# Optimization experiments

Hardware: AMD Instinct MI355X
Metric: run time of the kernel (lower is better)

The kernel has to match this reference:

```python
import jax, jax.numpy as jnp
import numpy as np

B, G, N, C = 8, 16, 1024, 256


def setup_inputs() -> dict:
    key = jax.random.key(0)
    k1, k2, k3, k4, k5 = jax.random.split(key, 5)
    x = jax.random.normal(k1, (B, G, N, C), dtype=jnp.float32)
    vs = jax.random.normal(k2, (B, G, 1, N, 3), dtype=jnp.float32)
    s = 1.0 / np.sqrt(C)
    W_fc = jax.random.normal(k3, (C, C), dtype=jnp.float32) * s   # nn.Linear weight [out,in]
    b_fc = jax.random.normal(k4, (C,), dtype=jnp.float32) * s
    W_vn = jax.random.normal(k5, (C, C), dtype=jnp.float32) * s   # VNLinear weight [out,in], no bias
    return {"x": x, "vs": vs, "W_fc": W_fc, "b_fc": b_fc, "W_vn": W_vn}


def reference(x, vs, W_fc, b_fc, W_vn):
    # q = fc(x): [B,G,N,C]
    q = jnp.einsum('bgnc,oc->bgno', x, W_fc) + b_fc
    # softmax over the point dim N (torch dim=2)
    atten = jax.nn.softmax(q, axis=2)
    xw = atten * x  # [B,G,N,C]
    # torch: expand to [B,G,C,N,3] * vs then sum over N.
    # Equivalent contraction without materializing the 5D tensor:
    v = jnp.squeeze(vs, axis=2)  # [B,G,N,3]
    out = jnp.einsum('bgnc,bgnd->bgcd', xw, v)  # [B,G,C,3]
    # VNLinear: bias-free linear over channel dim, shared across the 3 vector comps
    return jnp.einsum('bgcd,oc->bgod', out, W_vn)  # [B,G,C,3]
```

## Files before the change

### kernel.cpp

```cpp
#include <hip/hip_runtime.h>
#include <hip/hip_bf16.h>


#define NQ 1024
#define CQ 256
#define RT 64
#define XS2 264
#define WB_OFF 131072

typedef __attribute__((ext_vector_type(8))) short bf16x8;
typedef __attribute__((ext_vector_type(4))) float f32x4;

__device__ __forceinline__ ushort2 pk2(float a, float b) {
    __hip_bfloat162 h = __float22bfloat162_rn(make_float2(a, b));
    ushort2 r;
    __builtin_memcpy(&r, &h, sizeof(r));
    return r;
}
__device__ __forceinline__ float bf2f(ushort h) {
    union { unsigned u; float f; } v; v.u = ((unsigned)h) << 16;
    return v.f;
}

__device__ __forceinline__ void bar_lgkm() {
    __builtin_amdgcn_sched_barrier(0);
    asm volatile("s_waitcnt lgkmcnt(0)" ::: "memory");
    __builtin_amdgcn_sched_barrier(0);
    __builtin_amdgcn_s_barrier();
    __builtin_amdgcn_sched_barrier(0);
}

__global__ __launch_bounds__(256)
void wfc_cvt(const float* __restrict__ Wfc, ushort* __restrict__ WbT) {
    const int i = blockIdx.x * 256 + threadIdx.x;
    const int o = i >> 6;
    const int k4 = (i & 63) * 4;
    float4 v = *reinterpret_cast<const float4*>(Wfc + (size_t)o * CQ + k4);
    ushort2 a0 = pk2(v.x, v.y), a1 = pk2(v.z, v.w);
    ushort4 pk = { a0.x, a0.y, a1.x, a1.y };
    *reinterpret_cast<ushort4*>(WbT + ((size_t)(k4 >> 3) * CQ + o) * 8 + (k4 & 7)) = pk;
}

__global__ __launch_bounds__(512, 4)
void attn_pool_partial(const float* __restrict__ x, const float* __restrict__ vs,
                       const ushort* __restrict__ WbT, float* __restrict__ ws) {
    __shared__ __align__(16) ushort xs[RT * XS2];
    __shared__ __align__(16) float  vsm[RT * 3];

    const int t = threadIdx.x;
    const int id = blockIdx.x;
    const int bg = id >> 4;
    const int nt = id & 15;
    const int n0 = nt * RT;

    const int w = t >> 6, lane = t & 63;
    const int quad = lane >> 4, l16 = lane & 15;
    const int bcol0 = w * 32 + l16;

    const float* xb = x + (size_t)bg * NQ * CQ;
    const float* vb = vs + (size_t)bg * NQ * 3;

    const bool vload = (t < 48);
    float4 vreg;
    if (vload) vreg = reinterpret_cast<const float4*>(vb + (size_t)n0 * 3)[t];
    __builtin_amdgcn_sched_barrier(0);

    float4 LA[8];
    #pragma unroll
    for (int p = 0; p < 8; ++p) {
        const int idx = p * 512 + t;
        const int row = idx >> 6, k4 = idx & 63;
        LA[p] = *reinterpret_cast<const float4*>(
            xb + (size_t)(n0 + row) * CQ + k4 * 4);
    }
    __builtin_amdgcn_sched_barrier(0);

    bf16x8 Bf0[8], Bf1[8];
    #pragma unroll
    for (int ks = 0; ks < 8; ++ks) {
        const size_t fo = (size_t)(ks * 4 + quad) * (CQ * 8);
        Bf0[ks] = *reinterpret_cast<const bf16x8*>(WbT + fo + (size_t)bcol0 * 8);
        Bf1[ks] = *reinterpret_cast<const bf16x8*>(WbT + fo + (size_t)(bcol0 + 16) * 8);
    }
    __builtin_amdgcn_sched_barrier(0);

    #pragma unroll
    for (int p = 0; p < 8; ++p) {
        const int idx = p * 512 + t;
        const int row = idx >> 6, k4 = idx & 63;
        ushort2 a0 = pk2(LA[p].x, LA[p].y), a1 = pk2(LA[p].z, LA[p].w);
        ushort4 pk = { a0.x, a0.y, a1.x, a1.y };
        *reinterpret_cast<ushort4*>(&xs[row * XS2 + k4 * 4]) = pk;
    }
    if (vload) reinterpret_cast<float4*>(vsm)[t] = vreg;

    bar_lgkm();

    f32x4 acc[4][2];
    #pragma unroll
    for (int m = 0; m < 4; ++m)
        #pragma unroll
        for (int ci = 0; ci < 2; ++ci) acc[m][ci] = (f32x4){0.f, 0.f, 0.f, 0.f};

    __builtin_amdgcn_s_setprio(1);
    #pragma unroll
    for (int ks = 0; ks < 8; ++ks) {
        const int kk = ks * 32 + quad * 8;
        #pragma unroll
        for (int m = 0; m < 4; ++m) {
            bf16x8 a = *reinterpret_cast<const bf16x8*>(&xs[(m * 16 + l16) * XS2 + kk]);
            acc[m][0] = __builtin_amdgcn_mfma_f32_16x16x32_bf16(a, Bf0[ks], acc[m][0], 0, 0, 0);
            acc[m][1] = __builtin_amdgcn_mfma_f32_16x16x32_bf16(a, Bf1[ks], acc[m][1], 0, 0, 0);
        }
    }
    __builtin_amdgcn_s_setprio(0);

    float rZ[2] = {0.f, 0.f}, rS0[2] = {0.f, 0.f}, rS1[2] = {0.f, 0.f}, rS2[2] = {0.f, 0.f};
    #pragma unroll
    for (int m = 0; m < 4; ++m) {
        const int rbase = m * 16 + quad * 4;
        float v0[4], v1[4], v2[4];
        #pragma unroll
        for (int r = 0; r < 4; ++r) {
            v0[r] = vsm[(rbase + r) * 3 + 0];
            v1[r] = vsm[(rbase + r) * 3 + 1];
            v2[r] = vsm[(rbase + r) * 3 + 2];
        }
        #pragma unroll
        for (int ci = 0; ci < 2; ++ci) {
            const int xc = w * 32 + ci * 16 + l16;
            #pragma unroll
            for (int r = 0; r < 4; ++r) {
                float e = __expf(acc[m][ci][r]);
                float xv = bf2f(xs[(rbase + r) * XS2 + xc]);
                rZ[ci] += e;
                float p = e * xv;
                rS0[ci] = fmaf(p, v0[r], rS0[ci]);
                rS1[ci] = fmaf(p, v1[r], rS1[ci]);
                rS2[ci] = fmaf(p, v2[r], rS2[ci]);
            }
        }
    }

    #pragma unroll
    for (int ci = 0; ci < 2; ++ci) {
        float z = rZ[ci], s0 = rS0[ci], s1 = rS1[ci], s2 = rS2[ci];
        #pragma unroll
        for (int off = 16; off < 64; off <<= 1) {
            z  += __shfl_xor(z,  off);
            s0 += __shfl_xor(s0, off);
            s1 += __shfl_xor(s1, off);
            s2 += __shfl_xor(s2, off);
        }
        if (quad == 0) {
            const int col = w * 32 + ci * 16 + l16;
            float* p = ws + ((size_t)bg * CQ + col) * 4;
            atomicAdd(&p[0], z);
            atomicAdd(&p[1], s0);
            atomicAdd(&p[2], s1);
            atomicAdd(&p[3], s2);
        }
    }
}

__global__ __launch_bounds__(256, 4)
void vn_linear(const float* __restrict__ ws, const float* __restrict__ Wvn,
               float* __restrict__ out) {
    __shared__ float Tsm[CQ][3];
    const int bg = blockIdx.x, t = threadIdx.x;
    {
        f32x4 z4 = *reinterpret_cast<const f32x4*>(ws + ((size_t)bg * CQ + t) * 4);
        float inv = 1.f / z4[0];
        Tsm[t][0] = z4[1] * inv;
        Tsm[t][1] = z4[2] * inv;
        Tsm[t][2] = z4[3] * inv;
    }
    __syncthreads();
    const float* wr = Wvn + (size_t)t * CQ;
    float a0 = 0.f, a1 = 0.f, a2 = 0.f;
    #pragma unroll
    for (int c = 0; c < CQ; c += 4) {
        float4 w4 = *reinterpret_cast<const float4*>(wr + c);
        a0 += w4.x * Tsm[c + 0][0] + w4.y * Tsm[c + 1][0]
            + w4.z * Tsm[c + 2][0] + w4.w * Tsm[c + 3][0];
        a1 += w4.x * Tsm[c + 0][1] + w4.y * Tsm[c + 1][1]
            + w4.z * Tsm[c + 2][1] + w4.w * Tsm[c + 3][1];
        a2 += w4.x * Tsm[c + 0][2] + w4.y * Tsm[c + 1][2]
            + w4.z * Tsm[c + 2][2] + w4.w * Tsm[c + 3][2];
    }
    float* op = out + ((size_t)bg * CQ + t) * 3;
    op[0] = a0; op[1] = a1; op[2] = a2;
}

extern "C" void kernel_launch(void* const* d_in, const int* in_sizes, int n_in,
                              void* d_out, int out_size, void* d_ws, size_t ws_size,
                              hipStream_t stream) {
    const float* x   = (const float*)d_in[0];
    const float* vs  = (const float*)d_in[1];
    const float* Wfc = (const float*)d_in[2];
    const float* Wvn = (const float*)d_in[4];
    float* out = (float*)d_out;
    float* ws  = (float*)d_ws;

    ushort* WbT = (ushort*)(ws + WB_OFF);

    (void)hipMemsetAsync(ws, 0, (size_t)128 * CQ * 4 * sizeof(float), stream);
    wfc_cvt<<<dim3(64), dim3(256), 0, stream>>>(Wfc, WbT);
    attn_pool_partial<<<dim3(2048), dim3(512), 0, stream>>>(x, vs, WbT, ws);
    vn_linear<<<dim3(128), dim3(256), 0, stream>>>(ws, Wvn, out);
}
```

Before: 217.1 us.

## Double-buffer x tiles in LDS and process four row tiles per block

Each block now handles four 64-row tiles of one (b,g) instead of one, with a double-buffered LDS staging area. The next tile's global loads are issued in two halves interleaved with the MFMA and softmax work on the current tile, so memory latency overlaps compute. The W_fc fragments are loaded into registers once per block rather than once per tile, and atomics drop by a factor of four. The trade-off is fewer blocks (512) and doubled LDS, which may reduce occupancy and the latency hiding that came from having many resident blocks.

```diff
diff --git a/kernel.cpp b/kernel.cpp
--- a/kernel.cpp
+++ b/kernel.cpp
@@ -44,36 +44,23 @@
 __global__ __launch_bounds__(512, 4)
 void attn_pool_partial(const float* __restrict__ x, const float* __restrict__ vs,
                        const ushort* __restrict__ WbT, float* __restrict__ ws) {
-    __shared__ __align__(16) ushort xs[RT * XS2];
-    __shared__ __align__(16) float  vsm[RT * 3];
+    __shared__ __align__(16) ushort xs[2][RT * XS2];
+    __shared__ __align__(16) float  vsm[2][RT * 3];
 
     const int t = threadIdx.x;
     const int id = blockIdx.x;
-    const int bg = id >> 4;
-    const int nt = id & 15;
-    const int n0 = nt * RT;
+    const int bg = id >> 2;
+    const int ntg = id & 3;
+    const int nb = ntg * 4 * RT;
 
     const int w = t >> 6, lane = t & 63;
     const int quad = lane >> 4, l16 = lane & 15;
     const int bcol0 = w * 32 + l16;
+    const bool vload = (t < 48);
 
     const float* xb = x + (size_t)bg * NQ * CQ;
     const float* vb = vs + (size_t)bg * NQ * 3;
 
-    const bool vload = (t < 48);
-    float4 vreg;
-    if (vload) vreg = reinterpret_cast<const float4*>(vb + (size_t)n0 * 3)[t];
-    __builtin_amdgcn_sched_barrier(0);
-
-    float4 LA[8];
-    #pragma unroll
-    for (int p = 0; p < 8; ++p) {
-        const int idx = p * 512 + t;
-        const int row = idx >> 6, k4 = idx & 63;
-        LA[p] = *reinterpret_cast<const float4*>(
-            xb + (size_t)(n0 + row) * CQ + k4 * 4);
-    }
-    __builtin_amdgcn_sched_barrier(0);
 
     bf16x8 Bf0[8], Bf1[8];
     #pragma unroll
@@ -84,61 +71,171 @@
     }
     __builtin_amdgcn_sched_barrier(0);
 
+    {
+        float4 vreg;
+        if (vload) vreg = reinterpret_cast<const float4*>(vb + (size_t)nb * 3)[t];
+        float4 L[8];
+        #pragma unroll
+        for (int p = 0; p < 8; ++p) {
+            const int row = p * 8 + w;
+            L[p] = *reinterpret_cast<const float4*>(
+                xb + (size_t)(nb + row) * CQ + lane * 4);
+        }
+        __builtin_amdgcn_sched_barrier(0);
+        #pragma unroll
+        for (int p = 0; p < 8; ++p) {
+            const int row = p * 8 + w;
+            ushort2 a0 = pk2(L[p].x, L[p].y), a1 = pk2(L[p].z, L[p].w);
+            ushort4 pk = { a0.x, a0.y, a1.x, a1.y };
+            *reinterpret_cast<ushort4*>(&xs[0][row * XS2 + lane * 4]) = pk;
+        }
+        if (vload) reinterpret_cast<float4*>(vsm[0])[t] = vreg;
+    }
+    bar_lgkm();
+
+    float rZ[2] = {0.f, 0.f}, rS0[2] = {0.f, 0.f}, rS1[2] = {0.f, 0.f}, rS2[2] = {0.f, 0.f};
+
     #pragma unroll
-    for (int p = 0; p < 8; ++p) {
-        const int idx = p * 512 + t;
-        const int row = idx >> 6, k4 = idx & 63;
-        ushort2 a0 = pk2(LA[p].x, LA[p].y), a1 = pk2(LA[p].z, LA[p].w);
-        ushort4 pk = { a0.x, a0.y, a1.x, a1.y };
-        *reinterpret_cast<ushort4*>(&xs[row * XS2 + k4 * 4]) = pk;
-    }
-    if (vload) reinterpret_cast<float4*>(vsm)[t] = vreg;
-
-    bar_lgkm();
-
-    f32x4 acc[4][2];
-    #pragma unroll
-    for (int m = 0; m < 4; ++m)
-        #pragma unroll
-        for (int ci = 0; ci < 2; ++ci) acc[m][ci] = (f32x4){0.f, 0.f, 0.f, 0.f};
-
-    __builtin_amdgcn_s_setprio(1);
-    #pragma unroll
-    for (int ks = 0; ks < 8; ++ks) {
-        const int kk = ks * 32 + quad * 8;
-        #pragma unroll
-        for (int m = 0; m < 4; ++m) {
-            bf16x8 a = *reinterpret_cast<const bf16x8*>(&xs[(m * 16 + l16) * XS2 + kk]);
-            acc[m][0] = __builtin_amdgcn_mfma_f32_16x16x32_bf16(a, Bf0[ks], acc[m][0], 0, 0, 0);
-            acc[m][1] = __builtin_amdgcn_mfma_f32_16x16x32_bf16(a, Bf1[ks], acc[m][1], 0, 0, 0);
-        }
-    }
-    __builtin_amdgcn_s_setprio(0);
-
-    float rZ[2] = {0.f, 0.f}, rS0[2] = {0.f, 0.f}, rS1[2] = {0.f, 0.f}, rS2[2] = {0.f, 0.f};
-    #pragma unroll
-    for (int m = 0; m < 4; ++m) {
-        const int rbase = m * 16 + quad * 4;
-        float v0[4], v1[4], v2[4];
-        #pragma unroll
-        for (int r = 0; r < 4; ++r) {
-            v0[r] = vsm[(rbase + r) * 3 + 0];
-            v1[r] = vsm[(rbase + r) * 3 + 1];
-            v2[r] = vsm[(rbase + r) * 3 + 2];
-        }
-        #pragma unroll
-        for (int ci = 0; ci < 2; ++ci) {
-            const int xc = w * 32 + ci * 16 + l16;
-            #pragma unroll
-            for (int r = 0; r < 4; ++r) {
-                float e = __expf(acc[m][ci][r]);
-                float xv = bf2f(xs[(rbase + r) * XS2 + xc]);
-                rZ[ci] += e;
-                float p = e * xv;
-                rS0[ci] = fmaf(p, v0[r], rS0[ci]);
-                rS1[ci] = fmaf(p, v1[r], rS1[ci]);
-                rS2[ci] = fmaf(p, v2[r], rS2[ci]);
-            }
+    for (int i = 0; i < 4; ++i) {
+        const int cur = i & 1, nxt = cur ^ 1;
+        const bool pf = (i < 3);
+        const size_t nnb = (size_t)(nb + (i + 1) * RT);
+
+        float4 LAa[4], LAb[4], vreg;
+        if (pf) {
+            if (vload) vreg = reinterpret_cast<const float4*>(vb + nnb * 3)[t];
+            #pragma unroll
+            for (int p = 0; p < 4; ++p) {
+                const int row = p * 8 + w;
+                LAa[p] = *reinterpret_cast<const float4*>(
+                    xb + (nnb + row) * CQ + lane * 4);
+            }
+        }
+        __builtin_amdgcn_sched_barrier(0);
+
+        {
+            f32x4 acc[2][2];
+            #pragma unroll
+            for (int mi = 0; mi < 2; ++mi)
+                #pragma unroll
+                for (int ci = 0; ci < 2; ++ci) acc[mi][ci] = (f32x4){0.f, 0.f, 0.f, 0.f};
+            __builtin_amdgcn_s_setprio(1);
+            #pragma unroll
+            for (int ks = 0; ks < 8; ++ks) {
+                const int kk = ks * 32 + quad * 8;
+                #pragma unroll
+                for (int mi = 0; mi < 2; ++mi) {
+                    bf16x8 a = *reinterpret_cast<const bf16x8*>(
+                        &xs[cur][(mi * 16 + l16) * XS2 + kk]);
+                    acc[mi][0] = __builtin_amdgcn_mfma_f32_16x16x32_bf16(a, Bf0[ks], acc[mi][0], 0, 0, 0);
+                    acc[mi][1] = __builtin_amdgcn_mfma_f32_16x16x32_bf16(a, Bf1[ks], acc[mi][1], 0, 0, 0);
+                }
+            }
+            __builtin_amdgcn_s_setprio(0);
+            #pragma unroll
+            for (int mi = 0; mi < 2; ++mi) {
+                const int rbase = mi * 16 + quad * 4;
+                float v0[4], v1[4], v2[4];
+                #pragma unroll
+                for (int r = 0; r < 4; ++r) {
+                    v0[r] = vsm[cur][(rbase + r) * 3 + 0];
+                    v1[r] = vsm[cur][(rbase + r) * 3 + 1];
+                    v2[r] = vsm[cur][(rbase + r) * 3 + 2];
+                }
+                #pragma unroll
+                for (int ci = 0; ci < 2; ++ci) {
+                    const int xc = w * 32 + ci * 16 + l16;
+                    #pragma unroll
+                    for (int r = 0; r < 4; ++r) {
+                        float e = __expf(acc[mi][ci][r]);
+                        float xv = bf2f(xs[cur][(rbase + r) * XS2 + xc]);
+                        rZ[ci] += e;
+                        float p = e * xv;
+                        rS0[ci] = fmaf(p, v0[r], rS0[ci]);
+                        rS1[ci] = fmaf(p, v1[r], rS1[ci]);
+                        rS2[ci] = fmaf(p, v2[r], rS2[ci]);
+                    }
+                }
+            }
+        }
+
+        if (pf) {
+            #pragma unroll
+            for (int p = 0; p < 4; ++p) {
+                const int row = p * 8 + w;
+                ushort2 a0 = pk2(LAa[p].x, LAa[p].y), a1 = pk2(LAa[p].z, LAa[p].w);
+                ushort4 pk = { a0.x, a0.y, a1.x, a1.y };
+                *reinterpret_cast<ushort4*>(&xs[nxt][row * XS2 + lane * 4]) = pk;
+            }
+            if (vload) reinterpret_cast<float4*>(vsm[nxt])[t] = vreg;
+        }
+        __builtin_amdgcn_sched_barrier(0);
+
+        if (pf) {
+            #pragma unroll
+            for (int p = 0; p < 4; ++p) {
+                const int row = 32 + p * 8 + w;
+                LAb[p] = *reinterpret_cast<const float4*>(
+                    xb + (nnb + row) * CQ + lane * 4);
+            }
+        }
+        __builtin_amdgcn_sched_barrier(0);
+
+        {
+            f32x4 acc[2][2];
+            #pragma unroll
+            for (int mi = 0; mi < 2; ++mi)
+                #pragma unroll
+                for (int ci = 0; ci < 2; ++ci) acc[mi][ci] = (f32x4){0.f, 0.f, 0.f, 0.f};
+            __builtin_amdgcn_s_setprio(1);
+            #pragma unroll
+            for (int ks = 0; ks < 8; ++ks) {
+                const int kk = ks * 32 + quad * 8;
+                #pragma unroll
+                for (int mi = 0; mi < 2; ++mi) {
+                    bf16x8 a = *reinterpret_cast<const bf16x8*>(
+                        &xs[cur][((mi + 2) * 16 + l16) * XS2 + kk]);
+                    acc[mi][0] = __builtin_amdgcn_mfma_f32_16x16x32_bf16(a, Bf0[ks], acc[mi][0], 0, 0, 0);
+                    acc[mi][1] = __builtin_amdgcn_mfma_f32_16x16x32_bf16(a, Bf1[ks], acc[mi][1], 0, 0, 0);
+                }
+            }
+            __builtin_amdgcn_s_setprio(0);
+            #pragma unroll
+            for (int mi = 0; mi < 2; ++mi) {
+                const int rbase = (mi + 2) * 16 + quad * 4;
+                float v0[4], v1[4], v2[4];
+                #pragma unroll
+                for (int r = 0; r < 4; ++r) {
+                    v0[r] = vsm[cur][(rbase + r) * 3 + 0];
+                    v1[r] = vsm[cur][(rbase + r) * 3 + 1];
+                    v2[r] = vsm[cur][(rbase + r) * 3 + 2];
+                }
+                #pragma unroll
+                for (int ci = 0; ci < 2; ++ci) {
+                    const int xc = w * 32 + ci * 16 + l16;
+                    #pragma unroll
+                    for (int r = 0; r < 4; ++r) {
+                        float e = __expf(acc[mi][ci][r]);
+                        float xv = bf2f(xs[cur][(rbase + r) * XS2 + xc]);
+                        rZ[ci] += e;
+                        float p = e * xv;
+                        rS0[ci] = fmaf(p, v0[r], rS0[ci]);
+                        rS1[ci] = fmaf(p, v1[r], rS1[ci]);
+                        rS2[ci] = fmaf(p, v2[r], rS2[ci]);
+                    }
+                }
+            }
+        }
+
+        if (pf) {
+            #pragma unroll
+            for (int p = 0; p < 4; ++p) {
+                const int row = 32 + p * 8 + w;
+                ushort2 a0 = pk2(LAb[p].x, LAb[p].y), a1 = pk2(LAb[p].z, LAb[p].w);
+                ushort4 pk = { a0.x, a0.y, a1.x, a1.y };
+                *reinterpret_cast<ushort4*>(&xs[nxt][row * XS2 + lane * 4]) = pk;
+            }
+            bar_lgkm();
         }
     }
 
@@ -206,6 +303,6 @@
 
     (void)hipMemsetAsync(ws, 0, (size_t)128 * CQ * 4 * sizeof(float), stream);
     wfc_cvt<<<dim3(64), dim3(256), 0, stream>>>(Wfc, WbT);
-    attn_pool_partial<<<dim3(2048), dim3(512), 0, stream>>>(x, vs, WbT, ws);
+    attn_pool_partial<<<dim3(512), dim3(512), 0, stream>>>(x, vs, WbT, ws);
     vn_linear<<<dim3(128), dim3(256), 0, stream>>>(ws, Wvn, out);
 }
```

Result: slower. 368.8 us (+69.9%).

## Double-buffer x tiles via direct global-to-LDS loads in persistent blocks

Applied to the files above, without the earlier changes.

Each block now walks 8 tiles of 32 rows instead of handling one 64-row tile, so the grid shrinks from 2048 to 512 blocks. The x tiles are loaded as fp32 straight into LDS with global_load_lds into a double buffer, using an XOR swizzle, and are converted to bf16 when the MFMA operands are read. The goal is to overlap the HBM loads with compute, skip the register round trip, and load the W_fc fragments once per block rather than once per tile. In exchange it uses twice the LDS (fp32 staging), repeats the bf16 conversion inside the MFMA loop, and leaves fewer blocks to hide latency across the device.

```diff
diff --git a/kernel.cpp b/kernel.cpp
--- a/kernel.cpp
+++ b/kernel.cpp
@@ -4,8 +4,8 @@
 
 #define NQ 1024
 #define CQ 256
-#define RT 64
-#define XS2 264
+#define RT 32
+#define TILES 8
 #define WB_OFF 131072
 
 typedef __attribute__((ext_vector_type(8))) short bf16x8;
@@ -17,17 +17,11 @@
     __builtin_memcpy(&r, &h, sizeof(r));
     return r;
 }
-__device__ __forceinline__ float bf2f(ushort h) {
-    union { unsigned u; float f; } v; v.u = ((unsigned)h) << 16;
-    return v.f;
-}
-
-__device__ __forceinline__ void bar_lgkm() {
-    __builtin_amdgcn_sched_barrier(0);
-    asm volatile("s_waitcnt lgkmcnt(0)" ::: "memory");
-    __builtin_amdgcn_sched_barrier(0);
-    __builtin_amdgcn_s_barrier();
-    __builtin_amdgcn_sched_barrier(0);
+
+__device__ __forceinline__ void gload16(const float* g, float* l) {
+    __builtin_amdgcn_global_load_lds(
+        (const __attribute__((address_space(1))) unsigned int*)g,
+        (__attribute__((address_space(3))) unsigned int*)l, 16, 0, 0);
 }
 
 __global__ __launch_bounds__(256)
@@ -44,38 +38,24 @@
 __global__ __launch_bounds__(512, 4)
 void attn_pool_partial(const float* __restrict__ x, const float* __restrict__ vs,
                        const ushort* __restrict__ WbT, float* __restrict__ ws) {
-    __shared__ __align__(16) ushort xs[RT * XS2];
-    __shared__ __align__(16) float  vsm[RT * 3];
+    __shared__ __align__(16) float xsf[2][RT * CQ];
+    __shared__ __align__(16) float vsm[TILES * RT * 3];
 
     const int t = threadIdx.x;
     const int id = blockIdx.x;
-    const int bg = id >> 4;
-    const int nt = id & 15;
-    const int n0 = nt * RT;
+    const int bg = id >> 2;
+    const int ntg = id & 3;
+    const int nb = ntg * (TILES * RT);
 
     const int w = t >> 6, lane = t & 63;
     const int quad = lane >> 4, l16 = lane & 15;
-    const int bcol0 = w * 32 + l16;
+    const int sxA = (l16 & 7) << 2;
 
     const float* xb = x + (size_t)bg * NQ * CQ;
     const float* vb = vs + (size_t)bg * NQ * 3;
 
-    const bool vload = (t < 48);
-    float4 vreg;
-    if (vload) vreg = reinterpret_cast<const float4*>(vb + (size_t)n0 * 3)[t];
-    __builtin_amdgcn_sched_barrier(0);
-
-    float4 LA[8];
-    #pragma unroll
-    for (int p = 0; p < 8; ++p) {
-        const int idx = p * 512 + t;
-        const int row = idx >> 6, k4 = idx & 63;
-        LA[p] = *reinterpret_cast<const float4*>(
-            xb + (size_t)(n0 + row) * CQ + k4 * 4);
-    }
-    __builtin_amdgcn_sched_barrier(0);
-
     bf16x8 Bf0[8], Bf1[8];
+    const int bcol0 = w * 32 + l16;
     #pragma unroll
     for (int ks = 0; ks < 8; ++ks) {
         const size_t fo = (size_t)(ks * 4 + quad) * (CQ * 8);
@@ -84,62 +64,101 @@
     }
     __builtin_amdgcn_sched_barrier(0);
 
-    #pragma unroll
-    for (int p = 0; p < 8; ++p) {
-        const int idx = p * 512 + t;
-        const int row = idx >> 6, k4 = idx & 63;
-        ushort2 a0 = pk2(LA[p].x, LA[p].y), a1 = pk2(LA[p].z, LA[p].w);
-        ushort4 pk = { a0.x, a0.y, a1.x, a1.y };
-        *reinterpret_cast<ushort4*>(&xs[row * XS2 + k4 * 4]) = pk;
-    }
+    const bool vload = (t < 192);
+    float4 vreg;
+    if (vload) vreg = reinterpret_cast<const float4*>(vb + (size_t)nb * 3)[t];
+    __builtin_amdgcn_sched_barrier(0);
+
+    #pragma unroll
+    for (int p = 0; p < 4; ++p) {
+        const int row = p * 8 + w;
+        gload16(xb + (size_t)(nb + row) * CQ + (((lane * 4) ^ (w << 2))),
+                &xsf[0][row * CQ]);
+    }
+    __builtin_amdgcn_sched_barrier(0);
     if (vload) reinterpret_cast<float4*>(vsm)[t] = vreg;
-
-    bar_lgkm();
-
-    f32x4 acc[4][2];
-    #pragma unroll
-    for (int m = 0; m < 4; ++m)
-        #pragma unroll
-        for (int ci = 0; ci < 2; ++ci) acc[m][ci] = (f32x4){0.f, 0.f, 0.f, 0.f};
-
-    __builtin_amdgcn_s_setprio(1);
-    #pragma unroll
-    for (int ks = 0; ks < 8; ++ks) {
-        const int kk = ks * 32 + quad * 8;
-        #pragma unroll
-        for (int m = 0; m < 4; ++m) {
-            bf16x8 a = *reinterpret_cast<const bf16x8*>(&xs[(m * 16 + l16) * XS2 + kk]);
-            acc[m][0] = __builtin_amdgcn_mfma_f32_16x16x32_bf16(a, Bf0[ks], acc[m][0], 0, 0, 0);
-            acc[m][1] = __builtin_amdgcn_mfma_f32_16x16x32_bf16(a, Bf1[ks], acc[m][1], 0, 0, 0);
-        }
-    }
-    __builtin_amdgcn_s_setprio(0);
+    __builtin_amdgcn_sched_barrier(0);
+    asm volatile("s_waitcnt vmcnt(0) lgkmcnt(0)" ::: "memory");
+    __builtin_amdgcn_sched_barrier(0);
+    __builtin_amdgcn_s_barrier();
+    __builtin_amdgcn_sched_barrier(0);
 
     float rZ[2] = {0.f, 0.f}, rS0[2] = {0.f, 0.f}, rS1[2] = {0.f, 0.f}, rS2[2] = {0.f, 0.f};
-    #pragma unroll
-    for (int m = 0; m < 4; ++m) {
-        const int rbase = m * 16 + quad * 4;
-        float v0[4], v1[4], v2[4];
-        #pragma unroll
-        for (int r = 0; r < 4; ++r) {
-            v0[r] = vsm[(rbase + r) * 3 + 0];
-            v1[r] = vsm[(rbase + r) * 3 + 1];
-            v2[r] = vsm[(rbase + r) * 3 + 2];
-        }
-        #pragma unroll
-        for (int ci = 0; ci < 2; ++ci) {
-            const int xc = w * 32 + ci * 16 + l16;
+
+    for (int i = 0; i < TILES; ++i) {
+        const int cur = i & 1;
+        const float* xsb = xsf[cur];
+
+        if (i < TILES - 1) {
+            const size_t gr = (size_t)(nb + (i + 1) * RT);
+            float* dst = xsf[cur ^ 1];
+            #pragma unroll
+            for (int p = 0; p < 4; ++p) {
+                const int row = p * 8 + w;
+                gload16(xb + (gr + row) * CQ + (((lane * 4) ^ (w << 2))),
+                        dst + row * CQ);
+            }
+        }
+        __builtin_amdgcn_sched_barrier(0);
+
+        f32x4 acc[2][2];
+        #pragma unroll
+        for (int mi = 0; mi < 2; ++mi)
+            #pragma unroll
+            for (int ci = 0; ci < 2; ++ci) acc[mi][ci] = (f32x4){0.f, 0.f, 0.f, 0.f};
+
+        __builtin_amdgcn_s_setprio(1);
+        #pragma unroll
+        for (int ks = 0; ks < 8; ++ks) {
+            const int kk = ks * 32 + quad * 8;
+            #pragma unroll
+            for (int mi = 0; mi < 2; ++mi) {
+                const int row = mi * 16 + l16;
+                float4 h0 = *reinterpret_cast<const float4*>(&xsb[row * CQ + (kk ^ sxA)]);
+                float4 h1 = *reinterpret_cast<const float4*>(&xsb[row * CQ + ((kk + 4) ^ sxA)]);
+                ushort2 p0 = pk2(h0.x, h0.y), p1 = pk2(h0.z, h0.w);
+                ushort2 p2 = pk2(h1.x, h1.y), p3 = pk2(h1.z, h1.w);
+                bf16x8 a = (bf16x8){ (short)p0.x, (short)p0.y, (short)p1.x, (short)p1.y,
+                                     (short)p2.x, (short)p2.y, (short)p3.x, (short)p3.y };
+                acc[mi][0] = __builtin_amdgcn_mfma_f32_16x16x32_bf16(a, Bf0[ks], acc[mi][0], 0, 0, 0);
+                acc[mi][1] = __builtin_amdgcn_mfma_f32_16x16x32_bf16(a, Bf1[ks], acc[mi][1], 0, 0, 0);
+            }
+        }
+        __builtin_amdgcn_s_setprio(0);
+
+        const float* vt = vsm + (size_t)(i * RT) * 3;
+        #pragma unroll
+        for (int mi = 0; mi < 2; ++mi) {
+            const int rbase = mi * 16 + quad * 4;
+            float v0[4], v1[4], v2[4];
             #pragma unroll
             for (int r = 0; r < 4; ++r) {
-                float e = __expf(acc[m][ci][r]);
-                float xv = bf2f(xs[(rbase + r) * XS2 + xc]);
-                rZ[ci] += e;
-                float p = e * xv;
-                rS0[ci] = fmaf(p, v0[r], rS0[ci]);
-                rS1[ci] = fmaf(p, v1[r], rS1[ci]);
-                rS2[ci] = fmaf(p, v2[r], rS2[ci]);
-            }
-        }
+                v0[r] = vt[(rbase + r) * 3 + 0];
+                v1[r] = vt[(rbase + r) * 3 + 1];
+                v2[r] = vt[(rbase + r) * 3 + 2];
+            }
+            #pragma unroll
+            for (int ci = 0; ci < 2; ++ci) {
+                const int xc = w * 32 + ci * 16 + l16;
+                #pragma unroll
+                for (int r = 0; r < 4; ++r) {
+                    const int row = rbase + r;
+                    float e = __expf(acc[mi][ci][r]);
+                    float xv = xsb[row * CQ + (xc ^ ((row & 7) << 2))];
+                    rZ[ci] += e;
+                    float p = e * xv;
+                    rS0[ci] = fmaf(p, v0[r], rS0[ci]);
+                    rS1[ci] = fmaf(p, v1[r], rS1[ci]);
+                    rS2[ci] = fmaf(p, v2[r], rS2[ci]);
+                }
+            }
+        }
+
+        __builtin_amdgcn_sched_barrier(0);
+        asm volatile("s_waitcnt vmcnt(0)" ::: "memory");
+        __builtin_amdgcn_sched_barrier(0);
+        __builtin_amdgcn_s_barrier();
+        __builtin_amdgcn_sched_barrier(0);
     }
 
     #pragma unroll
@@ -206,6 +225,6 @@
 
     (void)hipMemsetAsync(ws, 0, (size_t)128 * CQ * 4 * sizeof(float), stream);
     wfc_cvt<<<dim3(64), dim3(256), 0, stream>>>(Wfc, WbT);
-    attn_pool_partial<<<dim3(2048), dim3(512), 0, stream>>>(x, vs, WbT, ws);
+    attn_pool_partial<<<dim3(512), dim3(512), 0, stream>>>(x, vs, WbT, ws);
     vn_linear<<<dim3(128), dim3(256), 0, stream>>>(ws, Wvn, out);
 }
```

Result: slower. 313.8 us (+44.6%).
